# Optimization experiments

Measured on AMD Instinct MI355X. Metric: run time of the kernel, lower is better.

Reference implementation:

```python
import jax, jax.numpy as jnp
import numpy as np

K = 512   # num_embeddings
D = 64    # embedding_dim
N = 262144

def l2norm(t, eps=1e-12):
    # matches F.normalize(t, p=2, dim=1)
    n = jnp.linalg.norm(t, axis=1, keepdims=True)
    return t / jnp.maximum(n, eps)

def setup_inputs() -> dict:
    key = jax.random.key(0)
    k1, k2, k3 = jax.random.split(key, 3)
    inputs = jax.random.normal(k1, (N, D), dtype=jnp.float32)
    labels = jax.random.randint(k2, (N,), 0, K)
    embedding = jax.random.normal(k3, (K, D), dtype=jnp.float32)  # frozen codebook (orthogonal init in original; random is fine for a numeric baseline)
    return {"inputs": inputs, "labels": labels, "embedding": embedding}

def reference(inputs, labels, embedding):
    # cosine distance path with labels != None
    flat = inputs.reshape(-1, D)
    distances = l2norm(flat) @ l2norm(embedding).T            # [N, K]
    encoding_indices = jnp.argmax(distances, axis=1)[:, None]  # [N, 1]
    encodings = jax.nn.one_hot(encoding_indices[:, 0], K, dtype=flat.dtype)  # [N, K] one-hot scatter
    quantized = (encodings @ embedding).reshape(inputs.shape)  # [N, D]
    # commitment loss: 1 - cosine sim at the supervised label index
    closs = (1.0 - jnp.take_along_axis(distances, labels[:, None], axis=1)[:, 0]).mean()
    loss = closs
    # straight-through estimator
    quantized = inputs + jax.lax.stop_gradient(quantized - inputs)
    perplexity = jnp.asarray(1, dtype=jnp.int32)
    return (loss, quantized, perplexity, encodings, encoding_indices)
```

## Files before the change

### kernel.cpp

```cpp
#include <hip/hip_runtime.h>
#include <hip/hip_bf16.h>

#define D_DIM 64
#define K_EMB 512
#define BM    128
#define XTSTR 132
#define RCAP  32768

typedef float f2v __attribute__((ext_vector_type(2)));

static constexpr size_t WS_RLIST = 16;
static constexpr size_t WS_ENT   = WS_RLIST + (size_t)RCAP * 4;
static constexpr size_t WS_EN64  = WS_ENT + (size_t)D_DIM * K_EMB * 4;

__global__ void prep_kernel(const float* __restrict__ emb,
                            float* __restrict__ entT,
                            double* __restrict__ en64,
                            double* __restrict__ loss_acc,
                            int* __restrict__ rcount) {
    const int k = blockIdx.x;
    const int d = threadIdx.x;
    double e = (double)emb[k * D_DIM + d];
    double sq = e * e;
    #pragma unroll
    for (int off = 32; off >= 1; off >>= 1) sq += __shfl_xor(sq, off);
    double inv = 1.0 / fmax(sqrt(sq), 1e-12);
    double v = e * inv;
    en64[(size_t)k * D_DIM + d] = v;
    entT[(size_t)d * K_EMB + k] = (float)v;
    if (k == 0 && d == 0) { *loss_acc = 0.0; *rcount = 0; }
}

__global__ __launch_bounds__(256, 3)
void main_kernel(const float* __restrict__ x, const int* __restrict__ labels,
                 const float* __restrict__ emb,
                 const float* __restrict__ entT, const double* __restrict__ en64,
                 double* __restrict__ loss_acc, int* __restrict__ rcount,
                 int* __restrict__ rlist,
                 float* __restrict__ out_quant, float* __restrict__ out_enc,
                 float* __restrict__ out_idx, int Ntot) {
    __shared__ float  XsT[D_DIM][XTSTR];
    __shared__ float  xnrm[BM];
    __shared__ int    idxs[BM];
    __shared__ double lred[4];

    const int tid = threadIdx.x;
    const size_t row0 = (size_t)blockIdx.x * BM;

    #pragma unroll
    for (int i = 0; i < 8; ++i) {
        int f = tid + i * 256;
        int r = f >> 4;
        int d4 = (f & 15) << 2;
        float4 v = *reinterpret_cast<const float4*>(x + (row0 + r) * D_DIM + d4);
        XsT[d4 + 0][r] = v.x; XsT[d4 + 1][r] = v.y;
        XsT[d4 + 2][r] = v.z; XsT[d4 + 3][r] = v.w;
    }
    __syncthreads();

    {
        int r = tid >> 1, p = tid & 1;
        size_t row = row0 + r;
        int lab = labels[row];
        const double* el = en64 + (size_t)lab * D_DIM;
        double s2 = 0.0, dp = 0.0;
        #pragma unroll
        for (int j = 0; j < 32; ++j) {
            int d = p * 32 + j;
            double xv = (double)XsT[d][r];
            s2 = fma(xv, xv, s2);
            dp = fma(xv, el[d], dp);
        }
        s2 += __shfl_xor(s2, 1);
        dp += __shfl_xor(dp, 1);
        double contrib = 0.0;
        if (p == 0) {
            double nrm = sqrt(s2);
            xnrm[r] = (float)nrm;
            contrib = 1.0 - dp / fmax(nrm, 1e-12);
        }
        #pragma unroll
        for (int off = 32; off >= 1; off >>= 1) contrib += __shfl_xor(contrib, off);
        if ((tid & 63) == 0) lred[tid >> 6] = contrib;
    }
    __syncthreads();
    if (tid == 0) {
        double s = (lred[0] + lred[1]) + (lred[2] + lred[3]);
        atomicAdd(loss_acc, s / (double)Ntot);
    }

    const int kk0 = (tid & 7) * 8;
    const int r0  = (tid >> 3) * 4;

    float v1[4], v2[4];
    int   k1[4];
    #pragma unroll
    for (int i = 0; i < 4; ++i) { v1[i] = -1e30f; v2[i] = -1e30f; k1[i] = 0; }

    for (int c = 0; c < 8; ++c) {
        const float* eb = entT + c * 64 + kk0;

        float acc[4][8];
        #pragma unroll
        for (int i = 0; i < 4; ++i)
            #pragma unroll
            for (int j = 0; j < 8; ++j) acc[i][j] = 0.0f;

        #pragma unroll 4
        for (int d = 0; d < D_DIM; ++d) {
            float4 xv = *reinterpret_cast<const float4*>(&XsT[d][r0]);
            float4 e0 = *reinterpret_cast<const float4*>(eb + (size_t)d * K_EMB);
            float4 e1 = *reinterpret_cast<const float4*>(eb + (size_t)d * K_EMB + 4);
            float xr[4] = {xv.x, xv.y, xv.z, xv.w};
            float ev[8] = {e0.x, e0.y, e0.z, e0.w, e1.x, e1.y, e1.z, e1.w};
            #pragma unroll
            for (int i = 0; i < 4; ++i)
                #pragma unroll
                for (int j = 0; j < 8; ++j)
                    acc[i][j] = fmaf(xr[i], ev[j], acc[i][j]);
        }

        const int kbase = c * 64 + kk0;
        #pragma unroll
        for (int i = 0; i < 4; ++i) {
            #pragma unroll
            for (int j = 0; j < 8; ++j) {
                float v = acc[i][j];
                int kk = kbase + j;
                bool better = (v > v1[i]);
                v2[i] = better ? v1[i] : fmaxf(v2[i], v);
                k1[i] = better ? kk : k1[i];
                v1[i] = better ? v : v1[i];
            }
        }
    }

    #pragma unroll
    for (int off = 4; off >= 1; off >>= 1) {
        #pragma unroll
        for (int i = 0; i < 4; ++i) {
            float ov1 = __shfl_xor(v1[i], off);
            float ov2 = __shfl_xor(v2[i], off);
            int   ok1 = __shfl_xor(k1[i], off);
            bool takeB = (ov1 > v1[i]) || (ov1 == v1[i] && ok1 < k1[i]);
            float n2 = takeB ? fmaxf(v1[i], ov2) : fmaxf(ov1, v2[i]);
            v1[i] = takeB ? ov1 : v1[i];
            k1[i] = takeB ? ok1 : k1[i];
            v2[i] = n2;
        }
    }

    if ((tid & 7) == 0) {
        #pragma unroll
        for (int i = 0; i < 4; ++i) {
            int r = r0 + i;
            idxs[r] = k1[i];
            float margin = 1e-4f * xnrm[r] + 1e-7f;
            if (v1[i] - v2[i] < margin) {
                int slot = atomicAdd(rcount, 1);
                if (slot < RCAP) rlist[slot] = (int)(row0 + r);
            }
        }
    }
    __syncthreads();

    if (tid < BM) out_idx[row0 + tid] = (float)idxs[tid];

    #pragma unroll 4
    for (int i = 0; i < 32; ++i) {
        int f = tid + i * 256;
        int r = f >> 6;
        int d = f & 63;
        int kq = idxs[r];
        float q = emb[(size_t)kq * D_DIM + d];
        float xv = XsT[d][r];
        __builtin_nontemporal_store(xv + (q - xv), out_quant + (row0 + r) * D_DIM + d);
    }

    for (int i = 0; i < BM; ++i) {
        int kq = idxs[i];
        int k = tid * 2;
        f2v o;
        o.x = (k     == kq) ? 1.0f : 0.0f;
        o.y = (k + 1 == kq) ? 1.0f : 0.0f;
        __builtin_nontemporal_store(o, (f2v*)(out_enc + (row0 + i) * K_EMB + k));
    }
}

__global__ void refine_kernel(const float* __restrict__ x, const float* __restrict__ emb,
                              const double* __restrict__ en64,
                              const int* __restrict__ rcount, const int* __restrict__ rlist,
                              float* __restrict__ out_quant, float* __restrict__ out_enc,
                              float* __restrict__ out_idx) {
    int cnt = *rcount; if (cnt > RCAP) cnt = RCAP;
    const int lane = threadIdx.x & 63;
    const int wave = (blockIdx.x * blockDim.x + threadIdx.x) >> 6;
    const int nwaves = (gridDim.x * blockDim.x) >> 6;
    for (int s = wave; s < cnt; s += nwaves) {
        int row = rlist[s];
        const float* xr = x + (size_t)row * D_DIM;
        double best = -1e300; int bestk = 0;
        for (int j = 0; j < 8; ++j) {
            int k = j * 64 + lane;
            const double* e = en64 + (size_t)k * D_DIM;
            double acc = 0.0;
            #pragma unroll
            for (int d = 0; d < D_DIM; ++d)
                acc = fma((double)xr[d], e[d], acc);
            if (acc > best || (acc == best && k < bestk)) { best = acc; bestk = k; }
        }
        #pragma unroll
        for (int off = 32; off >= 1; off >>= 1) {
            double ov = __shfl_xor(best, off);
            int    ok = __shfl_xor(bestk, off);
            if (ov > best || (ov == best && ok < bestk)) { best = ov; bestk = ok; }
        }
        int old = (int)(out_idx[row] + 0.5f);
        if (bestk != old) {
            if (lane == 0) {
                out_idx[row] = (float)bestk;
                out_enc[(size_t)row * K_EMB + old]   = 0.0f;
                out_enc[(size_t)row * K_EMB + bestk] = 1.0f;
            }
            float q = emb[(size_t)bestk * D_DIM + lane];
            float xv = xr[lane];
            out_quant[(size_t)row * D_DIM + lane] = xv + (q - xv);
        }
    }
}

__global__ void final_kernel(const double* __restrict__ loss_acc,
                             float* __restrict__ out_loss,
                             float* __restrict__ out_perp) {
    if (threadIdx.x == 0) {
        out_loss[0] = (float)(*loss_acc);
        out_perp[0] = 1.0f;
    }
}

extern "C" void kernel_launch(void* const* d_in, const int* in_sizes, int n_in,
                              void* d_out, int out_size, void* d_ws, size_t ws_size,
                              hipStream_t stream) {
    const float* x      = (const float*)d_in[0];
    const int*   labels = (const int*)d_in[1];
    const float* emb    = (const float*)d_in[2];
    const int Ntot = in_sizes[0] / D_DIM;

    char* ws = (char*)d_ws;
    double* loss_acc = (double*)(ws);
    int*    rcount   = (int*)(ws + 8);
    int*    rlist    = (int*)(ws + WS_RLIST);
    float*  entT     = (float*)(ws + WS_ENT);
    double* en64     = (double*)(ws + WS_EN64);

    float* out       = (float*)d_out;
    float* out_loss  = out;
    float* out_quant = out + 1;
    float* out_perp  = out + 1 + (size_t)Ntot * D_DIM;
    float* out_enc   = out + 2 + (size_t)Ntot * D_DIM;
    float* out_idx   = out_enc + (size_t)Ntot * K_EMB;

    hipLaunchKernelGGL(prep_kernel, dim3(K_EMB), dim3(D_DIM), 0, stream,
                       emb, entT, en64, loss_acc, rcount);
    hipLaunchKernelGGL(main_kernel, dim3(Ntot / BM), dim3(256), 0, stream,
                       x, labels, emb, entT, en64, loss_acc, rcount, rlist,
                       out_quant, out_enc, out_idx, Ntot);
    hipLaunchKernelGGL(refine_kernel, dim3(128), dim3(256), 0, stream,
                       x, emb, en64, rcount, rlist, out_quant, out_enc, out_idx);
    hipLaunchKernelGGL(final_kernel, dim3(1), dim3(64), 0, stream,
                       loss_acc, out_loss, out_perp);
}
```

Measured before the change: 946.6 us.

## Zero one-hot output in a separate fill kernel and scatter ones

Moves the dense one-hot encoding write out of the main kernel into a dedicated kernel that streams 16-byte nontemporal zero stores over the whole buffer. The main kernel then writes only the single 1.0 per row. The main kernel is also reshaped to 512 threads per block with two rows per thread, and the loss and quantized-output loops are remapped to match. This trades one extra kernel launch and a separate pass for a wider, simpler store stream in place of 8-byte stores interleaved with compute.

```diff
diff --git a/kernel.cpp b/kernel.cpp
--- a/kernel.cpp
+++ b/kernel.cpp
@@ -8,6 +8,7 @@
 #define RCAP  32768
 
 typedef float f2v __attribute__((ext_vector_type(2)));
+typedef float f4v __attribute__((ext_vector_type(4)));
 
 static constexpr size_t WS_RLIST = 16;
 static constexpr size_t WS_ENT   = WS_RLIST + (size_t)RCAP * 4;
@@ -31,7 +32,20 @@
     if (k == 0 && d == 0) { *loss_acc = 0.0; *rcount = 0; }
 }
 
-__global__ __launch_bounds__(256, 3)
+__global__ void zero_enc_kernel(float* __restrict__ out_enc, size_t total) {
+    const size_t n4 = (total - 4) >> 2;
+    f4v* __restrict__ p4 = (f4v*)(out_enc + 2);
+    const size_t stride = (size_t)gridDim.x * blockDim.x;
+    f4v z; z.x = 0.f; z.y = 0.f; z.z = 0.f; z.w = 0.f;
+    for (size_t i = (size_t)blockIdx.x * blockDim.x + threadIdx.x; i < n4; i += stride)
+        __builtin_nontemporal_store(z, p4 + i);
+    if (blockIdx.x == 0 && threadIdx.x == 0) {
+        out_enc[0] = 0.f; out_enc[1] = 0.f;
+        out_enc[total - 2] = 0.f; out_enc[total - 1] = 0.f;
+    }
+}
+
+__global__ __launch_bounds__(512, 6)
 void main_kernel(const float* __restrict__ x, const int* __restrict__ labels,
                  const float* __restrict__ emb,
                  const float* __restrict__ entT, const double* __restrict__ en64,
@@ -42,14 +56,14 @@
     __shared__ float  XsT[D_DIM][XTSTR];
     __shared__ float  xnrm[BM];
     __shared__ int    idxs[BM];
-    __shared__ double lred[4];
+    __shared__ double lred[8];
 
     const int tid = threadIdx.x;
     const size_t row0 = (size_t)blockIdx.x * BM;
 
     #pragma unroll
-    for (int i = 0; i < 8; ++i) {
-        int f = tid + i * 256;
+    for (int i = 0; i < 4; ++i) {
+        int f = tid + i * 512;
         int r = f >> 4;
         int d4 = (f & 15) << 2;
         float4 v = *reinterpret_cast<const float4*>(x + (row0 + r) * D_DIM + d4);
@@ -59,20 +73,19 @@
     __syncthreads();
 
     {
-        int r = tid >> 1, p = tid & 1;
-        size_t row = row0 + r;
-        int lab = labels[row];
+        int r = tid >> 2, p = tid & 3;
+        int lab = labels[row0 + r];
         const double* el = en64 + (size_t)lab * D_DIM;
         double s2 = 0.0, dp = 0.0;
         #pragma unroll
-        for (int j = 0; j < 32; ++j) {
-            int d = p * 32 + j;
+        for (int j = 0; j < 16; ++j) {
+            int d = p * 16 + j;
             double xv = (double)XsT[d][r];
             s2 = fma(xv, xv, s2);
             dp = fma(xv, el[d], dp);
         }
-        s2 += __shfl_xor(s2, 1);
-        dp += __shfl_xor(dp, 1);
+        s2 += __shfl_xor(s2, 1); s2 += __shfl_xor(s2, 2);
+        dp += __shfl_xor(dp, 1); dp += __shfl_xor(dp, 2);
         double contrib = 0.0;
         if (p == 0) {
             double nrm = sqrt(s2);
@@ -85,36 +98,38 @@
     }
     __syncthreads();
     if (tid == 0) {
-        double s = (lred[0] + lred[1]) + (lred[2] + lred[3]);
+        double s = 0.0;
+        #pragma unroll
+        for (int w = 0; w < 8; ++w) s += lred[w];
         atomicAdd(loss_acc, s / (double)Ntot);
     }
 
     const int kk0 = (tid & 7) * 8;
-    const int r0  = (tid >> 3) * 4;
-
-    float v1[4], v2[4];
-    int   k1[4];
-    #pragma unroll
-    for (int i = 0; i < 4; ++i) { v1[i] = -1e30f; v2[i] = -1e30f; k1[i] = 0; }
+    const int r0  = (tid >> 3) * 2;
+
+    float v1[2], v2[2];
+    int   k1[2];
+    #pragma unroll
+    for (int i = 0; i < 2; ++i) { v1[i] = -1e30f; v2[i] = -1e30f; k1[i] = 0; }
 
     for (int c = 0; c < 8; ++c) {
         const float* eb = entT + c * 64 + kk0;
 
-        float acc[4][8];
-        #pragma unroll
-        for (int i = 0; i < 4; ++i)
+        float acc[2][8];
+        #pragma unroll
+        for (int i = 0; i < 2; ++i)
             #pragma unroll
             for (int j = 0; j < 8; ++j) acc[i][j] = 0.0f;
 
         #pragma unroll 4
         for (int d = 0; d < D_DIM; ++d) {
-            float4 xv = *reinterpret_cast<const float4*>(&XsT[d][r0]);
+            f2v xv = *reinterpret_cast<const f2v*>(&XsT[d][r0]);
             float4 e0 = *reinterpret_cast<const float4*>(eb + (size_t)d * K_EMB);
             float4 e1 = *reinterpret_cast<const float4*>(eb + (size_t)d * K_EMB + 4);
-            float xr[4] = {xv.x, xv.y, xv.z, xv.w};
+            float xr[2] = {xv.x, xv.y};
             float ev[8] = {e0.x, e0.y, e0.z, e0.w, e1.x, e1.y, e1.z, e1.w};
             #pragma unroll
-            for (int i = 0; i < 4; ++i)
+            for (int i = 0; i < 2; ++i)
                 #pragma unroll
                 for (int j = 0; j < 8; ++j)
                     acc[i][j] = fmaf(xr[i], ev[j], acc[i][j]);
@@ -122,7 +137,7 @@
 
         const int kbase = c * 64 + kk0;
         #pragma unroll
-        for (int i = 0; i < 4; ++i) {
+        for (int i = 0; i < 2; ++i) {
             #pragma unroll
             for (int j = 0; j < 8; ++j) {
                 float v = acc[i][j];
@@ -138,7 +153,7 @@
     #pragma unroll
     for (int off = 4; off >= 1; off >>= 1) {
         #pragma unroll
-        for (int i = 0; i < 4; ++i) {
+        for (int i = 0; i < 2; ++i) {
             float ov1 = __shfl_xor(v1[i], off);
             float ov2 = __shfl_xor(v2[i], off);
             int   ok1 = __shfl_xor(k1[i], off);
@@ -152,7 +167,7 @@
 
     if ((tid & 7) == 0) {
         #pragma unroll
-        for (int i = 0; i < 4; ++i) {
+        for (int i = 0; i < 2; ++i) {
             int r = r0 + i;
             idxs[r] = k1[i];
             float margin = 1e-4f * xnrm[r] + 1e-7f;
@@ -164,26 +179,22 @@
     }
     __syncthreads();
 
-    if (tid < BM) out_idx[row0 + tid] = (float)idxs[tid];
+    if (tid < BM) {
+        out_idx[row0 + tid] = (float)idxs[tid];
+        out_enc[(row0 + tid) * (size_t)K_EMB + idxs[tid]] = 1.0f;
+    }
 
     #pragma unroll 4
-    for (int i = 0; i < 32; ++i) {
-        int f = tid + i * 256;
-        int r = f >> 6;
-        int d = f & 63;
+    for (int i = 0; i < 16; ++i) {
+        int f = i * 512 + tid;
+        int dl = f & 15;
+        int r  = (f >> 4) & 127;
+        int dg = f >> 11;
+        int d  = dg * 16 + dl;
         int kq = idxs[r];
         float q = emb[(size_t)kq * D_DIM + d];
         float xv = XsT[d][r];
         __builtin_nontemporal_store(xv + (q - xv), out_quant + (row0 + r) * D_DIM + d);
-    }
-
-    for (int i = 0; i < BM; ++i) {
-        int kq = idxs[i];
-        int k = tid * 2;
-        f2v o;
-        o.x = (k     == kq) ? 1.0f : 0.0f;
-        o.y = (k + 1 == kq) ? 1.0f : 0.0f;
-        __builtin_nontemporal_store(o, (f2v*)(out_enc + (row0 + i) * K_EMB + k));
     }
 }
 
@@ -262,7 +273,9 @@
 
     hipLaunchKernelGGL(prep_kernel, dim3(K_EMB), dim3(D_DIM), 0, stream,
                        emb, entT, en64, loss_acc, rcount);
-    hipLaunchKernelGGL(main_kernel, dim3(Ntot / BM), dim3(256), 0, stream,
+    hipLaunchKernelGGL(zero_enc_kernel, dim3(2048), dim3(256), 0, stream,
+                       out_enc, (size_t)Ntot * K_EMB);
+    hipLaunchKernelGGL(main_kernel, dim3(Ntot / BM), dim3(512), 0, stream,
                        x, labels, emb, entT, en64, loss_acc, rcount, rlist,
                        out_quant, out_enc, out_idx, Ntot);
     hipLaunchKernelGGL(refine_kernel, dim3(128), dim3(256), 0, stream,
```

Result: slower. 1.398 ms (+47.7%).

## Move one-hot encoding writes into a separate 16-byte aligned store kernel

Applied to the files above, without the earlier changes.

The one-hot encodings output is no longer written inside main_kernel. main_kernel now stores int indices to a workspace buffer, and a new grid-stride enc_kernel writes the 512 MB encodings matrix with aligned 16-byte nontemporal stores. The output starts at a 2-float offset, so the kernel shifts by two floats and patches row boundaries and the two ends separately. This targets misaligned 8-byte stores and the store traffic that limited main_kernel's occupancy, at the cost of an extra launch and an idx buffer round trip. refine_kernel still runs after enc_kernel and overwrites the rows it corrects.

```diff
diff --git a/kernel.cpp b/kernel.cpp
--- a/kernel.cpp
+++ b/kernel.cpp
@@ -8,10 +8,12 @@
 #define RCAP  32768
 
 typedef float f2v __attribute__((ext_vector_type(2)));
+typedef float f4v __attribute__((ext_vector_type(4)));
 
 static constexpr size_t WS_RLIST = 16;
 static constexpr size_t WS_ENT   = WS_RLIST + (size_t)RCAP * 4;
 static constexpr size_t WS_EN64  = WS_ENT + (size_t)D_DIM * K_EMB * 4;
+static constexpr size_t WS_IDX   = WS_EN64 + (size_t)K_EMB * D_DIM * 8;
 
 __global__ void prep_kernel(const float* __restrict__ emb,
                             float* __restrict__ entT,
@@ -36,9 +38,9 @@
                  const float* __restrict__ emb,
                  const float* __restrict__ entT, const double* __restrict__ en64,
                  double* __restrict__ loss_acc, int* __restrict__ rcount,
-                 int* __restrict__ rlist,
-                 float* __restrict__ out_quant, float* __restrict__ out_enc,
-                 float* __restrict__ out_idx, int Ntot) {
+                 int* __restrict__ rlist, int* __restrict__ idx32,
+                 float* __restrict__ out_quant, float* __restrict__ out_idx,
+                 int Ntot) {
     __shared__ float  XsT[D_DIM][XTSTR];
     __shared__ float  xnrm[BM];
     __shared__ int    idxs[BM];
@@ -164,7 +166,10 @@
     }
     __syncthreads();
 
-    if (tid < BM) out_idx[row0 + tid] = (float)idxs[tid];
+    if (tid < BM) {
+        out_idx[row0 + tid] = (float)idxs[tid];
+        idx32[row0 + tid]   = idxs[tid];
+    }
 
     #pragma unroll 4
     for (int i = 0; i < 32; ++i) {
@@ -176,14 +181,42 @@
         float xv = XsT[d][r];
         __builtin_nontemporal_store(xv + (q - xv), out_quant + (row0 + r) * D_DIM + d);
     }
-
-    for (int i = 0; i < BM; ++i) {
-        int kq = idxs[i];
-        int k = tid * 2;
-        f2v o;
-        o.x = (k     == kq) ? 1.0f : 0.0f;
-        o.y = (k + 1 == kq) ? 1.0f : 0.0f;
-        __builtin_nontemporal_store(o, (f2v*)(out_enc + (row0 + i) * K_EMB + k));
+}
+
+__global__ void enc_kernel(const int* __restrict__ idx32,
+                           float* __restrict__ out_enc, int Ntot) {
+    const size_t nslots = (((size_t)Ntot * K_EMB) - 4) >> 2;
+    f4v* __restrict__ p4 = (f4v*)(out_enc + 2);
+    const size_t stride = (size_t)gridDim.x * blockDim.x;
+    for (size_t j = (size_t)blockIdx.x * blockDim.x + threadIdx.x; j < nslots; j += stride) {
+        size_t flat = 2 + (j << 2);
+        int row = (int)(flat >> 9);
+        int c0  = (int)(flat & 511);
+        f4v o;
+        if (c0 <= 508) {
+            int idx = idx32[row];
+            o.x = (c0     == idx) ? 1.f : 0.f;
+            o.y = (c0 + 1 == idx) ? 1.f : 0.f;
+            o.z = (c0 + 2 == idx) ? 1.f : 0.f;
+            o.w = (c0 + 3 == idx) ? 1.f : 0.f;
+        } else {
+            int ia = idx32[row];
+            int ib = idx32[row + 1];
+            o.x = (ia == 510) ? 1.f : 0.f;
+            o.y = (ia == 511) ? 1.f : 0.f;
+            o.z = (ib == 0)   ? 1.f : 0.f;
+            o.w = (ib == 1)   ? 1.f : 0.f;
+        }
+        __builtin_nontemporal_store(o, p4 + j);
+    }
+    if (blockIdx.x == 0 && threadIdx.x == 0) {
+        int i0 = idx32[0];
+        out_enc[0] = (i0 == 0) ? 1.f : 0.f;
+        out_enc[1] = (i0 == 1) ? 1.f : 0.f;
+        size_t last = (size_t)Ntot * K_EMB;
+        int il = idx32[Ntot - 1];
+        out_enc[last - 2] = (il == 510) ? 1.f : 0.f;
+        out_enc[last - 1] = (il == 511) ? 1.f : 0.f;
     }
 }
 
@@ -252,6 +285,7 @@
     int*    rlist    = (int*)(ws + WS_RLIST);
     float*  entT     = (float*)(ws + WS_ENT);
     double* en64     = (double*)(ws + WS_EN64);
+    int*    idx32    = (int*)(ws + WS_IDX);
 
     float* out       = (float*)d_out;
     float* out_loss  = out;
@@ -264,7 +298,9 @@
                        emb, entT, en64, loss_acc, rcount);
     hipLaunchKernelGGL(main_kernel, dim3(Ntot / BM), dim3(256), 0, stream,
                        x, labels, emb, entT, en64, loss_acc, rcount, rlist,
-                       out_quant, out_enc, out_idx, Ntot);
+                       idx32, out_quant, out_idx, Ntot);
+    hipLaunchKernelGGL(enc_kernel, dim3(2048), dim3(256), 0, stream,
+                       idx32, out_enc, Ntot);
     hipLaunchKernelGGL(refine_kernel, dim3(128), dim3(256), 0, stream,
                        x, emb, en64, rcount, rlist, out_quant, out_enc, out_idx);
     hipLaunchKernelGGL(final_kernel, dim3(1), dim3(64), 0, stream,
```

Result: slower. 1.034 ms (+9.3%).
